# Performance work log

Hardware: AMD Instinct MI355X
Metric: run time of the kernel (lower is better)

Reference implementation:

```python
import jax, jax.numpy as jnp
import numpy as np

H = 256  # hidden_dim
N = 500000  # num_orbitals
M = 8192  # num_molecules


def setup_inputs() -> dict:
    key = jax.random.key(0)
    ks = jax.random.split(key, 12)
    s = lambda fan_in: 1.0 / np.sqrt(fan_in)
    inp = {
        "orbital_embeddings": jax.random.normal(ks[0], (N, H), dtype=jnp.float32),
        "batch": jnp.sort(jax.random.randint(ks[1], (N,), 0, M, dtype=jnp.int32)),
        "num_molecules": M,
        # attention MLP: Linear(H, H//2) -> ReLU -> Linear(H//2, 1)
        "aW1": jax.random.uniform(ks[2], (H, H // 2), jnp.float32, -s(H), s(H)),
        "ab1": jnp.zeros((H // 2,), jnp.float32),
        "aW2": jax.random.uniform(ks[3], (H // 2, 1), jnp.float32, -s(H // 2), s(H // 2)),
        "ab2": jnp.zeros((1,), jnp.float32),
        # global head: Linear(H,H)->ReLU->Linear(H,H//2)->ReLU->Linear(H//2,1)
        "gW1": jax.random.uniform(ks[4], (H, H), jnp.float32, -s(H), s(H)),
        "gb1": jnp.zeros((H,), jnp.float32),
        "gW2": jax.random.uniform(ks[5], (H, H // 2), jnp.float32, -s(H), s(H)),
        "gb2": jnp.zeros((H // 2,), jnp.float32),
        "gW3": jax.random.uniform(ks[6], (H // 2, 1), jnp.float32, -s(H // 2), s(H // 2)),
        "gb3": jnp.zeros((1,), jnp.float32),
    }
    return inp


def reference(orbital_embeddings, batch, num_molecules, aW1, ab1, aW2, ab2,
              gW1, gb1, gW2, gb2, gW3, gb3):
    # attention logits: [N, 1] (dropout is identity in eval mode)
    h = jax.nn.relu(orbital_embeddings @ aW1 + ab1)
    logits = h @ aW2 + ab2  # [N, 1]

    # per-molecule (segment) softmax over orbitals, numerically stable
    lg = logits[:, 0]  # [N]
    seg_max = jax.ops.segment_max(lg, batch, num_segments=num_molecules)  # [M]
    seg_max = jnp.where(jnp.isfinite(seg_max), seg_max, 0.0)  # empty segments
    ex = jnp.exp(lg - seg_max[batch])  # [N]
    denom = jax.ops.segment_sum(ex, batch, num_segments=num_molecules)  # [M]
    w = ex / denom[batch]  # [N]

    # weighted scatter-add pooling -> [M, H]
    weighted = orbital_embeddings * w[:, None]
    mol = jax.ops.segment_sum(weighted, batch, num_segments=num_molecules)

    # global head MLP -> [M, 1]
    g = jax.nn.relu(mol @ gW1 + gb1)
    g = jax.nn.relu(g @ gW2 + gb2)
    return g @ gW3 + gb3
```

## Files before the change

### kernel.cpp

```cpp
#include <hip/hip_runtime.h>
#include <hip/hip_bf16.h>

#define H      256
#define CAP    64
#define GRID12 512

typedef _Float16 f16x8 __attribute__((ext_vector_type(8)));
typedef float    f32x4 __attribute__((ext_vector_type(4)));

__global__ __launch_bounds__(256) void k0_pack(
    const float* __restrict__ aW1, const float* __restrict__ gW1,
    const float* __restrict__ gW2,
    _Float16* __restrict__ aW1F, float* __restrict__ gW1P, float* __restrict__ gW2P)
{
    int idx = blockIdx.x * 256 + threadIdx.x;
    int stride = gridDim.x * 256;
    for (int e8 = idx; e8 < 4096; e8 += stride) {
        int l = e8 & 63, kknt = e8 >> 6;
        int kk = kknt & 7, nt = kknt >> 3;
        int j = nt*16 + (l & 15);
        int kbase = kk*32 + (l >> 4)*8;
        f16x8 v;
        #pragma unroll
        for (int e = 0; e < 8; ++e) v[e] = (_Float16)aW1[(kbase + e)*128 + j];
        *reinterpret_cast<f16x8*>(aW1F + e8*8) = v;
    }
    for (int e = idx; e < 64*256*4; e += stride) {
        int s = e & 3, j = (e >> 2) & 255, kq = e >> 10;
        gW1P[e] = gW1[(kq*4+s)*256 + j];
    }
    for (int e = idx; e < 64*128*4; e += stride) {
        int s = e & 3, j = (e >> 2) & 127, kq = e >> 9;
        gW2P[e] = gW2[(kq*4+s)*128 + j];
    }
}

__global__ __launch_bounds__(256) void k2a_starts(
    const int* __restrict__ batch, int* __restrict__ starts, int N, int M)
{
    int i = blockIdx.x * 256 + threadIdx.x;
    if (i >= N) return;
    int b = batch[i];
    if (i == 0) {
        for (int m = 0; m <= b; ++m) starts[m] = 0;
    } else {
        int p = batch[i-1];
        for (int m = p + 1; m <= b; ++m) starts[m] = i;
    }
    if (i == N - 1) {
        for (int m = b + 1; m <= M; ++m) starts[m] = N;
    }
}

__global__ __launch_bounds__(256) void k12_fused(
    const float* __restrict__ emb, const int* __restrict__ starts,
    const _Float16* __restrict__ aW1F, const float* __restrict__ ab1,
    const float* __restrict__ aW2, const float* __restrict__ ab2,
    float* __restrict__ mol, int M)
{
    __shared__ __align__(16) _Float16 eh[CAP * H];
    __shared__ float pr[4][CAP];
    __shared__ float lgs[CAP];
    __shared__ float wl[CAP];

    const int t = threadIdx.x, w = t >> 6, l = t & 63;
    char* ldsb = reinterpret_cast<char*>(eh);
    const f32x4 zero = {0.f, 0.f, 0.f, 0.f};

    f16x8 bf[2][8];
    #pragma unroll
    for (int nt2 = 0; nt2 < 2; ++nt2)
        #pragma unroll
        for (int kk = 0; kk < 8; ++kk)
            bf[nt2][kk] = *reinterpret_cast<const f16x8*>(
                aW1F + (size_t)(((2*w + nt2)*8 + kk)*64 + l)*8);

    float b1v[2], w2v[2];
    #pragma unroll
    for (int nt2 = 0; nt2 < 2; ++nt2) {
        int j = 32*w + nt2*16 + (l & 15);
        b1v[nt2] = ab1[j];
        w2v[nt2] = aW2[j];
    }
    const float bo = ab2[0];

    int m = blockIdx.x, start = 0, end = 0;
    for (;;) {
        if (m >= M) return;
        start = starts[m]; end = starts[m + 1];
        if (start < end) break;
        mol[(size_t)m*H + t] = 0.f;
        m += GRID12;
    }

    int c0 = start;
    int cc = min(CAP, end - c0);
    float4 pv[16];

#define ISSUE(C0, CC) do {                                                      \
    _Pragma("unroll")                                                           \
    for (int j = 0; j < 8; ++j) {                                               \
        int ci = t + j*256;                                                     \
        int r = ci >> 5, c8 = ci & 31;                                          \
        int rr = r < (CC) ? r : (CC) - 1;                                       \
        const float4* pp = reinterpret_cast<const float4*>(                     \
            emb + (size_t)((C0) + rr)*H) + c8*2;                                \
        pv[2*j] = pp[0]; pv[2*j+1] = pp[1];                                     \
    } } while (0)

    ISSUE(c0, cc);
    float mx = -INFINITY, s = 0.f, acc = 0.f;

    for (;;) {
        const int  cur_m = m, cur_c0 = c0, cur_cc = cc;
        const bool last_chunk = (c0 + CAP >= end);

        __syncthreads();

        #pragma unroll
        for (int j = 0; j < 8; ++j) {
            int ci = t + j*256;
            int r = ci >> 5, c8 = ci & 31;
            float4 v0 = pv[2*j], v1 = pv[2*j+1];
            f16x8 hv;
            hv[0]=(_Float16)v0.x; hv[1]=(_Float16)v0.y; hv[2]=(_Float16)v0.z; hv[3]=(_Float16)v0.w;
            hv[4]=(_Float16)v1.x; hv[5]=(_Float16)v1.y; hv[6]=(_Float16)v1.z; hv[7]=(_Float16)v1.w;
            int wb = (r*512 + c8*16) ^ ((r & 7) << 4);
            *reinterpret_cast<f16x8*>(ldsb + wb) = hv;
        }

        int nm = m, nc0 = c0 + CAP, nend = end;
        bool have_next = true;
        if (last_chunk) {
            nm = m + GRID12;
            for (;;) {
                if (nm >= M) { have_next = false; break; }
                int ns = starts[nm], ne = starts[nm + 1];
                if (ns < ne) { nc0 = ns; nend = ne; break; }
                mol[(size_t)nm*H + t] = 0.f;
                nm += GRID12;
            }
        }
        int ncc = 0;
        if (have_next) { ncc = min(CAP, nend - nc0); ISSUE(nc0, ncc); }
        __syncthreads();

        #pragma unroll
        for (int rt = 0; rt < 4; ++rt) {
            int row   = rt*16 + (l & 15);
            int rbase = row*512 + (l >> 4)*16;
            int swz   = (row & 7) << 4;
            f32x4 a20 = zero, a21 = zero;
            #pragma unroll
            for (int kk = 0; kk < 8; ++kk) {
                f16x8 af = *reinterpret_cast<const f16x8*>(ldsb + ((rbase + kk*64) ^ swz));
                a20 = __builtin_amdgcn_mfma_f32_16x16x32_f16(af, bf[0][kk], a20, 0, 0, 0);
                a21 = __builtin_amdgcn_mfma_f32_16x16x32_f16(af, bf[1][kk], a21, 0, 0, 0);
            }
            #pragma unroll
            for (int r = 0; r < 4; ++r) {
                float h0 = a20[r] + b1v[0]; h0 = h0 > 0.f ? h0 : 0.f;
                float h1 = a21[r] + b1v[1]; h1 = h1 > 0.f ? h1 : 0.f;
                float p = h0*w2v[0] + h1*w2v[1];
                p += __shfl_xor(p, 1, 64);
                p += __shfl_xor(p, 2, 64);
                p += __shfl_xor(p, 4, 64);
                p += __shfl_xor(p, 8, 64);
                if ((l & 15) == 0) pr[w][rt*16 + (l >> 4)*4 + r] = p;
            }
        }
        __syncthreads();
        if (t < CAP) lgs[t] = pr[0][t] + pr[1][t] + pr[2][t] + pr[3][t] + bo;
        __syncthreads();

        float lg = (l < cur_cc) ? lgs[l] : -INFINITY;
        float mc = lg;
        mc = fmaxf(mc, __shfl_xor(mc, 1, 64));
        mc = fmaxf(mc, __shfl_xor(mc, 2, 64));
        mc = fmaxf(mc, __shfl_xor(mc, 4, 64));
        mc = fmaxf(mc, __shfl_xor(mc, 8, 64));
        mc = fmaxf(mc, __shfl_xor(mc, 16, 64));
        mc = fmaxf(mc, __shfl_xor(mc, 32, 64));
        float mxn = fmaxf(mx, mc);
        float rsc = __expf(mx - mxn);
        float e = (l < cur_cc) ? __expf(lg - mxn) : 0.f;
        float sc = e;
        sc += __shfl_xor(sc, 1, 64);
        sc += __shfl_xor(sc, 2, 64);
        sc += __shfl_xor(sc, 4, 64);
        sc += __shfl_xor(sc, 8, 64);
        sc += __shfl_xor(sc, 16, 64);
        sc += __shfl_xor(sc, 32, 64);
        s = s*rsc + sc;
        if (w == 0) wl[l] = e;
        mx = mxn;
        __syncthreads();

        acc *= rsc;
        const float* ebase = emb + (size_t)cur_c0*H + t;
        #pragma unroll 16
        for (int g = 0; g < CAP; ++g) {
            int rr = g < cur_cc ? g : cur_cc - 1;
            acc += wl[g] * ebase[(size_t)rr*H];
        }

        if (last_chunk) {
            mol[(size_t)cur_m*H + t] = acc / s;
            mx = -INFINITY; s = 0.f; acc = 0.f;
        }
        if (!have_next) return;
        m = nm; c0 = nc0; end = nend; cc = ncc;
    }
#undef ISSUE
}

__global__ __launch_bounds__(256) void k3_mlp(
    const float* __restrict__ mol, const float* __restrict__ gW1P,
    const float* __restrict__ gb1, const float* __restrict__ gW2P,
    const float* __restrict__ gb2, const float* __restrict__ gW3,
    const float* __restrict__ gb3, float* __restrict__ out, int M)
{
    __shared__ __align__(16) float mt[32 * 256];
    __shared__ __align__(16) float g1[32 * 256];
    __shared__ float tmp[4][16];
    int t = threadIdx.x;
    int blk = blockIdx.x;

    #pragma unroll
    for (int i = 0; i < 8; ++i) {
        int f = t + i*256;
        long gidx = (long)blk*2048 + f;
        float4 v = make_float4(0.f,0.f,0.f,0.f);
        if (gidx < (long)M*64) v = reinterpret_cast<const float4*>(mol)[gidx];
        reinterpret_cast<float4*>(mt)[f] = v;
    }
    __syncthreads();

    int j = t & 127, mh = t >> 7;

    float a0[16], a1[16];
    #pragma unroll
    for (int m = 0; m < 16; ++m) { a0[m] = 0.f; a1[m] = 0.f; }
    for (int kq = 0; kq < 64; ++kq) {
        float4 w0 = reinterpret_cast<const float4*>(gW1P)[kq*256 + j];
        float4 w1 = reinterpret_cast<const float4*>(gW1P)[kq*256 + j + 128];
        #pragma unroll
        for (int m = 0; m < 16; ++m) {
            float4 e = *reinterpret_cast<const float4*>(&mt[(mh*16 + m)*256 + kq*4]);
            a0[m] += e.x*w0.x + e.y*w0.y + e.z*w0.z + e.w*w0.w;
            a1[m] += e.x*w1.x + e.y*w1.y + e.z*w1.z + e.w*w1.w;
        }
    }
    {
        float b0 = gb1[j], b1 = gb1[j + 128];
        #pragma unroll
        for (int m = 0; m < 16; ++m) {
            float v0 = a0[m] + b0; v0 = v0 > 0.f ? v0 : 0.f;
            float v1 = a1[m] + b1; v1 = v1 > 0.f ? v1 : 0.f;
            g1[(mh*16 + m)*256 + j]       = v0;
            g1[(mh*16 + m)*256 + j + 128] = v1;
        }
    }
    __syncthreads();

    float a2[16];
    #pragma unroll
    for (int m = 0; m < 16; ++m) a2[m] = 0.f;
    for (int kq = 0; kq < 64; ++kq) {
        float4 w = reinterpret_cast<const float4*>(gW2P)[kq*128 + j];
        #pragma unroll
        for (int m = 0; m < 16; ++m) {
            float4 e = *reinterpret_cast<const float4*>(&g1[(mh*16 + m)*256 + kq*4]);
            a2[m] += e.x*w.x + e.y*w.y + e.z*w.z + e.w*w.w;
        }
    }

    float b2 = gb2[j], w3 = gW3[j];
    float p[16];
    #pragma unroll
    for (int m = 0; m < 16; ++m) {
        float v = a2[m] + b2; v = v > 0.f ? v : 0.f;
        p[m] = v * w3;
    }
    #pragma unroll
    for (int off = 32; off >= 1; off >>= 1) {
        #pragma unroll
        for (int m = 0; m < 16; ++m) p[m] += __shfl_xor(p[m], off, 64);
    }
    int wid = t >> 6;
    if ((t & 63) == 0) {
        #pragma unroll
        for (int m = 0; m < 16; ++m) tmp[wid][m] = p[m];
    }
    __syncthreads();
    if (t < 32) {
        int om = blk*32 + t;
        if (om < M) out[om] = tmp[(t >> 4)*2][t & 15] + tmp[(t >> 4)*2 + 1][t & 15] + gb3[0];
    }
}

extern "C" void kernel_launch(void* const* d_in, const int* in_sizes, int n_in,
                              void* d_out, int out_size, void* d_ws, size_t ws_size,
                              hipStream_t stream) {
    const float* emb  = (const float*)d_in[0];
    const int*   batch= (const int*)d_in[1];
    const float* aW1  = (const float*)d_in[3];
    const float* ab1  = (const float*)d_in[4];
    const float* aW2  = (const float*)d_in[5];
    const float* ab2  = (const float*)d_in[6];
    const float* gW1  = (const float*)d_in[7];
    const float* gb1  = (const float*)d_in[8];
    const float* gW2  = (const float*)d_in[9];
    const float* gb2  = (const float*)d_in[10];
    const float* gW3  = (const float*)d_in[11];
    const float* gb3  = (const float*)d_in[12];
    float* outp = (float*)d_out;

    int N = in_sizes[0] / H;
    int M = out_size;

    char* ws = (char*)d_ws;
    size_t off = 0;
    float*     mol    = (float*)(ws + off);    off += (8u<<20);
    _Float16*  aW1F   = (_Float16*)(ws + off); off += 65536;
    float*     gW1P   = (float*)(ws + off);    off += 262144;
    float*     gW2P   = (float*)(ws + off);    off += 131072;
    int*       starts = (int*)(ws + off);      off += (size_t)(M+1)*4;

    int g12 = M < GRID12 ? M : GRID12;

    k0_pack<<<64, 256, 0, stream>>>(aW1, gW1, gW2, aW1F, gW1P, gW2P);
    k2a_starts<<<(N + 255)/256, 256, 0, stream>>>(batch, starts, N, M);
    k12_fused<<<g12, 256, 0, stream>>>(emb, starts, aW1F, ab1, aW2, ab2, mol, M);
    k3_mlp<<<(M + 31)/32, 256, 0, stream>>>(mol, gW1P, gb1, gW2P, gb2, gW3, gb3, outp, M);
}
```

Before: 303.7 us.

## Pool from fp16 LDS tile instead of re-reading embeddings; double grid, cache segment starts

```diff
diff --git a/kernel.cpp b/kernel.cpp
--- a/kernel.cpp
+++ b/kernel.cpp
@@ -3,7 +3,9 @@
 
 #define H      256
 #define CAP    64
-#define GRID12 512
+#define GRID12 1024
+#define MMAX   16
+#define RPW    8
 
 typedef _Float16 f16x8 __attribute__((ext_vector_type(8)));
 typedef float    f32x4 __attribute__((ext_vector_type(4)));
@@ -52,7 +54,7 @@
     }
 }
 
-__global__ __launch_bounds__(256) void k12_fused(
+__global__ __launch_bounds__(256, 4) void k12_fused(
     const float* __restrict__ emb, const int* __restrict__ starts,
     const _Float16* __restrict__ aW1F, const float* __restrict__ ab1,
     const float* __restrict__ aW2, const float* __restrict__ ab2,
@@ -60,12 +62,18 @@
 {
     __shared__ __align__(16) _Float16 eh[CAP * H];
     __shared__ float pr[4][CAP];
-    __shared__ float lgs[CAP];
     __shared__ float wl[CAP];
+    __shared__ int   sst[2*MMAX];
 
     const int t = threadIdx.x, w = t >> 6, l = t & 63;
+    const int bid = blockIdx.x;
     char* ldsb = reinterpret_cast<char*>(eh);
     const f32x4 zero = {0.f, 0.f, 0.f, 0.f};
+
+    if (t < 2*MMAX) {
+        int idx = bid + (t >> 1)*GRID12 + (t & 1);
+        sst[t] = starts[idx <= M ? idx : M];
+    }
 
     f16x8 bf[2][8];
     #pragma unroll
@@ -84,13 +92,15 @@
     }
     const float bo = ab2[0];
 
-    int m = blockIdx.x, start = 0, end = 0;
+    __syncthreads();
+
+    int k = 0, start = 0, end = 0;
     for (;;) {
-        if (m >= M) return;
-        start = starts[m]; end = starts[m + 1];
+        if (k >= MMAX || bid + (size_t)k*GRID12 >= (size_t)M) return;
+        start = sst[2*k]; end = sst[2*k+1];
         if (start < end) break;
-        mol[(size_t)m*H + t] = 0.f;
-        m += GRID12;
+        mol[(size_t)(bid + k*GRID12)*H + t] = 0.f;
+        ++k;
     }
 
     int c0 = start;
@@ -112,7 +122,8 @@
     float mx = -INFINITY, s = 0.f, acc = 0.f;
 
     for (;;) {
-        const int  cur_m = m, cur_c0 = c0, cur_cc = cc;
+        const int  cur_m  = bid + k*GRID12;
+        const int  cur_cc = cc;
         const bool last_chunk = (c0 + CAP >= end);
 
         __syncthreads();
@@ -129,16 +140,16 @@
             *reinterpret_cast<f16x8*>(ldsb + wb) = hv;
         }
 
-        int nm = m, nc0 = c0 + CAP, nend = end;
+        int nk = k, nc0 = c0 + CAP, nend = end;
         bool have_next = true;
         if (last_chunk) {
-            nm = m + GRID12;
+            ++nk;
             for (;;) {
-                if (nm >= M) { have_next = false; break; }
-                int ns = starts[nm], ne = starts[nm + 1];
+                if (nk >= MMAX || bid + (size_t)nk*GRID12 >= (size_t)M) { have_next = false; break; }
+                int ns = sst[2*nk], ne = sst[2*nk+1];
                 if (ns < ne) { nc0 = ns; nend = ne; break; }
-                mol[(size_t)nm*H + t] = 0.f;
-                nm += GRID12;
+                mol[(size_t)(bid + nk*GRID12)*H + t] = 0.f;
+                ++nk;
             }
         }
         int ncc = 0;
@@ -170,10 +181,9 @@
             }
         }
         __syncthreads();
-        if (t < CAP) lgs[t] = pr[0][t] + pr[1][t] + pr[2][t] + pr[3][t] + bo;
-        __syncthreads();
-
-        float lg = (l < cur_cc) ? lgs[l] : -INFINITY;
+
+        float lg = -INFINITY;
+        if (l < cur_cc) lg = pr[0][l] + pr[1][l] + pr[2][l] + pr[3][l] + bo;
         float mc = lg;
         mc = fmaxf(mc, __shfl_xor(mc, 1, 64));
         mc = fmaxf(mc, __shfl_xor(mc, 2, 64));
@@ -192,16 +202,16 @@
         sc += __shfl_xor(sc, 16, 64);
         sc += __shfl_xor(sc, 32, 64);
         s = s*rsc + sc;
+        mx = mxn;
         if (w == 0) wl[l] = e;
-        mx = mxn;
         __syncthreads();
 
         acc *= rsc;
-        const float* ebase = emb + (size_t)cur_c0*H + t;
         #pragma unroll 16
         for (int g = 0; g < CAP; ++g) {
-            int rr = g < cur_cc ? g : cur_cc - 1;
-            acc += wl[g] * ebase[(size_t)rr*H];
+            _Float16 hv = *reinterpret_cast<const _Float16*>(
+                ldsb + ((g*512 + t*2) ^ ((g & 7) << 4)));
+            acc += wl[g] * (float)hv;
         }
 
         if (last_chunk) {
@@ -209,7 +219,7 @@
             mx = -INFINITY; s = 0.f; acc = 0.f;
         }
         if (!have_next) return;
-        m = nm; c0 = nc0; end = nend; cc = ncc;
+        k = nk; c0 = nc0; end = nend; cc = ncc;
     }
 #undef ISSUE
 }
```

Result: slower. 541.1 us (+78.2%).
